# Kernel tuning notes

Measured on AMD Instinct MI355X. Metric: run time of the kernel, lower is better.

## Reference

```python
import jax, jax.numpy as jnp
import numpy as np

N = 50000
E = 800000
NFEAT, NHID, NCLASS = 128, 128, 40


def setup_inputs() -> dict:
    key = jax.random.key(0)
    ks = jax.random.split(key, 8)
    x = jax.random.normal(ks[0], (N, NFEAT), dtype=jnp.float32)
    edge_index = jax.random.randint(ks[1], (2, E), 0, N, dtype=jnp.int64)
    def glorot(k, fan_in, fan_out):
        s = jnp.sqrt(6.0 / (fan_in + fan_out)).astype(jnp.float32)
        return jax.random.uniform(k, (fan_in, fan_out), jnp.float32, -s, s)
    W1 = glorot(ks[2], NFEAT, NHID); b1 = jnp.zeros((NHID,), jnp.float32)
    W2 = glorot(ks[3], NHID, NHID);  b2 = jnp.zeros((NHID,), jnp.float32)
    W3 = glorot(ks[4], NHID, NCLASS); b3 = jnp.zeros((NCLASS,), jnp.float32)
    return {"x": x, "edge_index": edge_index,
            "W1": W1, "b1": b1, "W2": W2, "b2": b2, "W3": W3, "b3": b3}


def _gcn_norm(edge_index, num_nodes, dtype):
    # Add self-loops, then symmetric normalization D^-1/2 (A+I) D^-1/2 (PyG gcn_norm).
    loop = jnp.arange(num_nodes, dtype=edge_index.dtype)
    src = jnp.concatenate([edge_index[0], loop])
    dst = jnp.concatenate([edge_index[1], loop])
    deg = jax.ops.segment_sum(jnp.ones_like(src, dtype=dtype), dst, num_segments=num_nodes)
    dinv = jnp.where(deg > 0, deg ** -0.5, 0.0).astype(dtype)
    norm = dinv[src] * dinv[dst]  # [E+N]
    return src, dst, norm


def _gcn_conv(h, src, dst, norm, W, b, num_nodes):
    h = h @ W                              # dense transform first (out_dim small)
    msg = h[src] * norm[:, None]           # gather + per-edge scale
    out = jax.ops.segment_sum(msg, dst, num_segments=num_nodes)  # scatter-add
    return out + b


def reference(x, edge_index, W1, b1, W2, b2, W3, b3):
    src, dst, norm = _gcn_norm(edge_index, N, x.dtype)
    h = jax.nn.relu(_gcn_conv(x, src, dst, norm, W1, b1, N))  # dropout: eval mode (identity)
    h = jax.nn.relu(_gcn_conv(h, src, dst, norm, W2, b2, N))
    h = _gcn_conv(h, src, dst, norm, W3, b3, N)
    return jax.nn.log_softmax(h, axis=-1)
```

## Files before the change

kernel.cpp:

```cpp
#include <hip/hip_runtime.h>
#include <stdint.h>

#define NN 50000
#define NE 800000

#define SWZ(j, k) ((j) * 128 + ((k) ^ (((j) & 7) << 2)))

__device__ inline unsigned short f2bf(float f) {
    union { float f; uint32_t u; } x; x.f = f;
    uint32_t u = x.u;
    return (unsigned short)((u + 0x7fffu + ((u >> 16) & 1u)) >> 16);
}
__device__ inline uint32_t pack2bf(float lo, float hi) {
    return (uint32_t)f2bf(lo) | ((uint32_t)f2bf(hi) << 16);
}
__device__ inline float bf2f(unsigned short h) {
    union { uint32_t u; float f; } c; c.u = ((uint32_t)h) << 16;
    return c.f;
}
__device__ inline float2 bfp2f2(uint32_t v) {
    union { uint32_t u; float f; } a, b;
    a.u = (v & 0xffffu) << 16;
    b.u = v & 0xffff0000u;
    return make_float2(a.f, b.f);
}

#define FMA4(ACC, S, B)                  \
    ACC.x = fmaf(S, B.x, ACC.x);         \
    ACC.y = fmaf(S, B.y, ACC.y);         \
    ACC.z = fmaf(S, B.z, ACC.z);         \
    ACC.w = fmaf(S, B.w, ACC.w);


__global__ void zero_i(int* p, int n) {
    int i = blockIdx.x * blockDim.x + threadIdx.x;
    if (i < n) p[i] = 0;
}

__global__ void hist_rank(const int* __restrict__ dst, int* hist, int* rank, int e) {
    int i = blockIdx.x * blockDim.x + threadIdx.x;
    if (i < e) rank[i] = atomicAdd(hist + dst[i], 1);
}

__global__ void dinv_k(const int* __restrict__ hist, float* dinv, int n) {
    int i = blockIdx.x * blockDim.x + threadIdx.x;
    if (i < n) dinv[i] = rsqrtf(1.0f + (float)hist[i]);
}

__global__ void scan1(const int* __restrict__ hist, int* row_ptr, int* bsum, int n) {
    __shared__ int s[256];
    int tid = threadIdx.x;
    int i = blockIdx.x * 256 + tid;
    int v = (i < n) ? hist[i] : 0;
    s[tid] = v;
    __syncthreads();
#pragma unroll
    for (int off = 1; off < 256; off <<= 1) {
        int y = (tid >= off) ? s[tid - off] : 0;
        __syncthreads();
        s[tid] += y;
        __syncthreads();
    }
    if (i < n) row_ptr[i] = s[tid] - v;
    if (tid == 255) bsum[blockIdx.x] = s[255];
}

__global__ void scan2(const int* __restrict__ bsum, int* boff, int nb) {
    __shared__ int s[256];
    int tid = threadIdx.x;
    int v = (tid < nb) ? bsum[tid] : 0;
    s[tid] = v;
    __syncthreads();
#pragma unroll
    for (int off = 1; off < 256; off <<= 1) {
        int y = (tid >= off) ? s[tid - off] : 0;
        __syncthreads();
        s[tid] += y;
        __syncthreads();
    }
    if (tid < nb) boff[tid] = s[tid] - v;
}

__global__ void scan3(int* row_ptr, const int* __restrict__ boff, int n) {
    int i = blockIdx.x * blockDim.x + threadIdx.x;
    if (i < n) row_ptr[i] += boff[i >> 8];
}

__global__ void bucket(const int* __restrict__ src, const int* __restrict__ dst,
                       const int* __restrict__ row_ptr, const int* __restrict__ rank,
                       int* __restrict__ csr_src, int e) {
    int i = blockIdx.x * blockDim.x + threadIdx.x;
    if (i < e) csr_src[row_ptr[dst[i]] + rank[i]] = src[i];
}


__global__ __launch_bounds__(256) void gemm128(const float* __restrict__ X,
                                               const float* __restrict__ W,
                                               const float* __restrict__ dinv,
                                               unsigned short* __restrict__ G, int n) {
    __shared__ float Ws[128 * 128];
    int t = threadIdx.x;
    int row0 = blockIdx.x * 128;

    const float4* Wv = (const float4*)W;
    float4* Wsv = (float4*)Ws;
#pragma unroll
    for (int i = 0; i < 16; i++) Wsv[t + i * 256] = Wv[t + i * 256];
    __syncthreads();

    int tx = t & 15;
    int ty = t >> 4;

    const float* xp[8];
#pragma unroll
    for (int ri = 0; ri < 8; ri++) {
        int row = row0 + ty + 16 * ri;
        int rowc = row < n ? row : n - 1;
        xp[ri] = X + (size_t)rowc * 128;
    }

    float4 acc0[8], acc1[8];
#pragma unroll
    for (int ri = 0; ri < 8; ri++) {
        acc0[ri] = make_float4(0.f, 0.f, 0.f, 0.f);
        acc1[ri] = make_float4(0.f, 0.f, 0.f, 0.f);
    }

#pragma unroll 2
    for (int k = 0; k < 128; k += 4) {
        float4 a[8];
#pragma unroll
        for (int ri = 0; ri < 8; ri++) a[ri] = *(const float4*)(xp[ri] + k);
        float4 b0[4], b1[4];
#pragma unroll
        for (int c = 0; c < 4; c++) {
            b0[c] = *(const float4*)(&Ws[(k + c) * 128 + 4 * tx]);
            b1[c] = *(const float4*)(&Ws[(k + c) * 128 + 64 + 4 * tx]);
        }
#pragma unroll
        for (int ri = 0; ri < 8; ri++) {
            FMA4(acc0[ri], a[ri].x, b0[0]);
            FMA4(acc0[ri], a[ri].y, b0[1]);
            FMA4(acc0[ri], a[ri].z, b0[2]);
            FMA4(acc0[ri], a[ri].w, b0[3]);
            FMA4(acc1[ri], a[ri].x, b1[0]);
            FMA4(acc1[ri], a[ri].y, b1[1]);
            FMA4(acc1[ri], a[ri].z, b1[2]);
            FMA4(acc1[ri], a[ri].w, b1[3]);
        }
    }

#pragma unroll
    for (int ri = 0; ri < 8; ri++) {
        int row = row0 + ty + 16 * ri;
        if (row >= n) continue;
        float di = dinv[row];
        uint2 o0, o1;
        o0.x = pack2bf(di * acc0[ri].x, di * acc0[ri].y);
        o0.y = pack2bf(di * acc0[ri].z, di * acc0[ri].w);
        o1.x = pack2bf(di * acc1[ri].x, di * acc1[ri].y);
        o1.y = pack2bf(di * acc1[ri].z, di * acc1[ri].w);
        *(uint2*)(&G[(size_t)row * 128 + 4 * tx]) = o0;
        *(uint2*)(&G[(size_t)row * 128 + 64 + 4 * tx]) = o1;
    }
}

__global__ __launch_bounds__(256) void gemm40(const float* __restrict__ X,
                                              const float* __restrict__ W,
                                              const float* __restrict__ dinv,
                                              unsigned short* __restrict__ G, int n) {
    __shared__ float WsT[40 * 128];
    int t = threadIdx.x;
    int row0 = blockIdx.x * 128;

    const float4* Wv = (const float4*)W;
#pragma unroll
    for (int i = 0; i < 5; i++) {
        int idx = t + i * 256;
        int k = idx / 10;
        int j4 = (idx - k * 10) * 4;
        float4 v = Wv[idx];
        WsT[(j4 + 0) * 128 + (k ^ (((j4 + 0) & 7) << 2))] = v.x;
        WsT[(j4 + 1) * 128 + (k ^ (((j4 + 1) & 7) << 2))] = v.y;
        WsT[(j4 + 2) * 128 + (k ^ (((j4 + 2) & 7) << 2))] = v.z;
        WsT[(j4 + 3) * 128 + (k ^ (((j4 + 3) & 7) << 2))] = v.w;
    }
    __syncthreads();

    int tx = t & 7;
    int ty = t >> 3;

    const float* xp[4];
#pragma unroll
    for (int ri = 0; ri < 4; ri++) {
        int row = row0 + ty + 32 * ri;
        int rowc = row < n ? row : n - 1;
        xp[ri] = X + (size_t)rowc * 128;
    }

    float acc[4][5];
#pragma unroll
    for (int ri = 0; ri < 4; ri++)
#pragma unroll
        for (int ci = 0; ci < 5; ci++) acc[ri][ci] = 0.f;

#pragma unroll 2
    for (int k = 0; k < 128; k += 4) {
        float4 a[4], b[5];
#pragma unroll
        for (int ri = 0; ri < 4; ri++) a[ri] = *(const float4*)(xp[ri] + k);
#pragma unroll
        for (int ci = 0; ci < 5; ci++) b[ci] = *(const float4*)(&WsT[SWZ(tx * 5 + ci, k)]);
#pragma unroll
        for (int ri = 0; ri < 4; ri++)
#pragma unroll
            for (int ci = 0; ci < 5; ci++) {
                acc[ri][ci] = fmaf(a[ri].x, b[ci].x, acc[ri][ci]);
                acc[ri][ci] = fmaf(a[ri].y, b[ci].y, acc[ri][ci]);
                acc[ri][ci] = fmaf(a[ri].z, b[ci].z, acc[ri][ci]);
                acc[ri][ci] = fmaf(a[ri].w, b[ci].w, acc[ri][ci]);
            }
    }

#pragma unroll
    for (int ri = 0; ri < 4; ri++) {
        int row = row0 + ty + 32 * ri;
        if (row >= n) continue;
        float di = dinv[row];
#pragma unroll
        for (int ci = 0; ci < 5; ci++)
            G[(size_t)row * 40 + tx * 5 + ci] = f2bf(di * acc[ri][ci]);
    }
}


__global__ __launch_bounds__(256) void aggregate128(const unsigned short* __restrict__ G,
                                                    const int* __restrict__ row_ptr,
                                                    const int* __restrict__ hist,
                                                    const int* __restrict__ csr_src,
                                                    const float* __restrict__ dinv,
                                                    const float* __restrict__ b,
                                                    float* __restrict__ Y, int n) {
    int node = blockIdx.x * 4 + (threadIdx.x >> 6);
    if (node >= n) return;
    int l = threadIdx.x & 63;
    const uint32_t* Gr = (const uint32_t*)G;

    float2 acc = bfp2f2(Gr[(size_t)node * 64 + l]);
    int p = row_ptr[node], p1 = p + hist[node];
    for (; p + 7 < p1; p += 8) {
        int s0 = csr_src[p],     s1 = csr_src[p + 1], s2 = csr_src[p + 2], s3 = csr_src[p + 3];
        int s4 = csr_src[p + 4], s5 = csr_src[p + 5], s6 = csr_src[p + 6], s7 = csr_src[p + 7];
        uint32_t v0 = Gr[(size_t)s0 * 64 + l], v1 = Gr[(size_t)s1 * 64 + l];
        uint32_t v2 = Gr[(size_t)s2 * 64 + l], v3 = Gr[(size_t)s3 * 64 + l];
        uint32_t v4 = Gr[(size_t)s4 * 64 + l], v5 = Gr[(size_t)s5 * 64 + l];
        uint32_t v6 = Gr[(size_t)s6 * 64 + l], v7 = Gr[(size_t)s7 * 64 + l];
        float2 f0 = bfp2f2(v0), f1 = bfp2f2(v1), f2 = bfp2f2(v2), f3 = bfp2f2(v3);
        float2 f4 = bfp2f2(v4), f5 = bfp2f2(v5), f6 = bfp2f2(v6), f7 = bfp2f2(v7);
        acc.x += ((f0.x + f1.x) + (f2.x + f3.x)) + ((f4.x + f5.x) + (f6.x + f7.x));
        acc.y += ((f0.y + f1.y) + (f2.y + f3.y)) + ((f4.y + f5.y) + (f6.y + f7.y));
    }
    for (; p + 3 < p1; p += 4) {
        int s0 = csr_src[p], s1 = csr_src[p + 1], s2 = csr_src[p + 2], s3 = csr_src[p + 3];
        float2 f0 = bfp2f2(Gr[(size_t)s0 * 64 + l]), f1 = bfp2f2(Gr[(size_t)s1 * 64 + l]);
        float2 f2 = bfp2f2(Gr[(size_t)s2 * 64 + l]), f3 = bfp2f2(Gr[(size_t)s3 * 64 + l]);
        acc.x += (f0.x + f1.x) + (f2.x + f3.x);
        acc.y += (f0.y + f1.y) + (f2.y + f3.y);
    }
    for (; p < p1; ++p) {
        float2 f = bfp2f2(Gr[(size_t)csr_src[p] * 64 + l]);
        acc.x += f.x; acc.y += f.y;
    }
    float di = dinv[node];
    float vx = fmaf(di, acc.x, b[2 * l]);
    float vy = fmaf(di, acc.y, b[2 * l + 1]);
    float2 o = make_float2(vx > 0.f ? vx : 0.f, vy > 0.f ? vy : 0.f);
    *(float2*)(Y + (size_t)node * 128 + 2 * l) = o;
}

__global__ __launch_bounds__(256) void aggregate40_lsm(const unsigned short* __restrict__ G,
                                                       const int* __restrict__ row_ptr,
                                                       const int* __restrict__ hist,
                                                       const int* __restrict__ csr_src,
                                                       const float* __restrict__ dinv,
                                                       const float* __restrict__ b,
                                                       float* __restrict__ Y, int n) {
    int node = blockIdx.x * 4 + (threadIdx.x >> 6);
    if (node >= n) return;
    int lane = threadIdx.x & 63;
    bool act = lane < 40;
    int lc = act ? lane : 0;
    float acc = act ? bf2f(G[(size_t)node * 40 + lane]) : 0.f;
    int p = row_ptr[node], p1 = p + hist[node];
    for (; p + 3 < p1; p += 4) {
        int s0 = csr_src[p], s1 = csr_src[p + 1], s2 = csr_src[p + 2], s3 = csr_src[p + 3];
        float f0 = bf2f(G[(size_t)s0 * 40 + lc]);
        float f1 = bf2f(G[(size_t)s1 * 40 + lc]);
        float f2 = bf2f(G[(size_t)s2 * 40 + lc]);
        float f3 = bf2f(G[(size_t)s3 * 40 + lc]);
        acc += (f0 + f1) + (f2 + f3);
    }
    for (; p < p1; ++p) acc += bf2f(G[(size_t)csr_src[p] * 40 + lc]);

    float v = act ? fmaf(dinv[node], acc, b[lane]) : -1e30f;
    float m = v;
#pragma unroll
    for (int off = 32; off > 0; off >>= 1) m = fmaxf(m, __shfl_xor(m, off, 64));
    float ex = act ? expf(v - m) : 0.f;
    float s_ = ex;
#pragma unroll
    for (int off = 32; off > 0; off >>= 1) s_ += __shfl_xor(s_, off, 64);
    float ls = logf(s_);
    if (act) Y[(size_t)node * 40 + lane] = v - m - ls;
}


extern "C" void kernel_launch(void* const* d_in, const int* in_sizes, int n_in,
                              void* d_out, int out_size, void* d_ws, size_t ws_size,
                              hipStream_t stream) {
    const float* x  = (const float*)d_in[0];
    const int*   ei = (const int*)d_in[1];
    const float* W1 = (const float*)d_in[2];
    const float* b1 = (const float*)d_in[3];
    const float* W2 = (const float*)d_in[4];
    const float* b2 = (const float*)d_in[5];
    const float* W3 = (const float*)d_in[6];
    const float* b3 = (const float*)d_in[7];
    float* out = (float*)d_out;

    const int n = NN, e = NE;
    const int* srcI = ei;
    const int* dstI = ei + e;

    char* ws = (char*)d_ws;
    int*   hist    = (int*)ws;
    float* dinv    = (float*)(ws + 200704);
    int*   row_ptr = (int*)(ws + 401408);
    int*   bsum    = (int*)(ws + 602112);
    int*   boff    = (int*)(ws + 603136);
    int*   rank    = (int*)(ws + 604160);
    int*   csr_src = (int*)(ws + 3804160);
    unsigned short* bufG = (unsigned short*)(ws + 7004160);
    float* bufA    = (float*)(ws + 7004160 + 12800000);

    int nb = (n + 255) / 256;

    zero_i<<<nb, 256, 0, stream>>>(hist, n);
    hist_rank<<<(e + 255) / 256, 256, 0, stream>>>(dstI, hist, rank, e);
    dinv_k<<<nb, 256, 0, stream>>>(hist, dinv, n);
    scan1<<<nb, 256, 0, stream>>>(hist, row_ptr, bsum, n);
    scan2<<<1, 256, 0, stream>>>(bsum, boff, nb);
    scan3<<<nb, 256, 0, stream>>>(row_ptr, boff, n);
    bucket<<<(e + 255) / 256, 256, 0, stream>>>(srcI, dstI, row_ptr, rank, csr_src, e);

    unsigned gg = (unsigned)((n + 127) / 128);
    unsigned ga = (unsigned)((n + 3) / 4);

    gemm128<<<gg, 256, 0, stream>>>(x, W1, dinv, bufG, n);
    aggregate128<<<ga, 256, 0, stream>>>(bufG, row_ptr, hist, csr_src, dinv, b1, bufA, n);
    gemm128<<<gg, 256, 0, stream>>>(bufA, W2, dinv, bufG, n);
    aggregate128<<<ga, 256, 0, stream>>>(bufG, row_ptr, hist, csr_src, dinv, b2, bufA, n);
    gemm40<<<gg, 256, 0, stream>>>(bufA, W3, dinv, bufG, n);
    aggregate40_lsm<<<ga, 256, 0, stream>>>(bufG, row_ptr, hist, csr_src, dinv, b3, out, n);
}
```

Baseline: 322.7 us.

## Gather neighbor rows with 16-byte loads across lane groups and fuse prep kernels

Aggregation for the 128-wide layers now splits each wave into four 16-lane groups. Each group gathers a different edge's full bf16 row with 16-byte vector loads, and the partial sums are reduced across groups with shuffles. The self-loop is folded in as edge zero. The dinv computation is merged into the first scan kernel, and the block-offset add of the third scan is folded into its consumers, removing two launches. This aims for wider memory transactions and more edges in flight, at the cost of extra shuffle reductions and more predicated work on low-degree nodes.

```diff
diff --git a/kernel.cpp b/kernel.cpp
--- a/kernel.cpp
+++ b/kernel.cpp
@@ -42,12 +42,8 @@
     if (i < e) rank[i] = atomicAdd(hist + dst[i], 1);
 }
 
-__global__ void dinv_k(const int* __restrict__ hist, float* dinv, int n) {
-    int i = blockIdx.x * blockDim.x + threadIdx.x;
-    if (i < n) dinv[i] = rsqrtf(1.0f + (float)hist[i]);
-}
-
-__global__ void scan1(const int* __restrict__ hist, int* row_ptr, int* bsum, int n) {
+__global__ void scan1(const int* __restrict__ hist, int* row_ptr, int* bsum,
+                      float* dinv, int n) {
     __shared__ int s[256];
     int tid = threadIdx.x;
     int i = blockIdx.x * 256 + tid;
@@ -61,7 +57,10 @@
         s[tid] += y;
         __syncthreads();
     }
-    if (i < n) row_ptr[i] = s[tid] - v;
+    if (i < n) {
+        row_ptr[i] = s[tid] - v;
+        dinv[i] = rsqrtf(1.0f + (float)v);
+    }
     if (tid == 255) bsum[blockIdx.x] = s[255];
 }
 
@@ -81,16 +80,14 @@
     if (tid < nb) boff[tid] = s[tid] - v;
 }
 
-__global__ void scan3(int* row_ptr, const int* __restrict__ boff, int n) {
+__global__ void bucket(const int* __restrict__ src, const int* __restrict__ dst,
+                       const int* __restrict__ row_ptr, const int* __restrict__ boff,
+                       const int* __restrict__ rank, int* __restrict__ csr_src, int e) {
     int i = blockIdx.x * blockDim.x + threadIdx.x;
-    if (i < n) row_ptr[i] += boff[i >> 8];
-}
-
-__global__ void bucket(const int* __restrict__ src, const int* __restrict__ dst,
-                       const int* __restrict__ row_ptr, const int* __restrict__ rank,
-                       int* __restrict__ csr_src, int e) {
-    int i = blockIdx.x * blockDim.x + threadIdx.x;
-    if (i < e) csr_src[row_ptr[dst[i]] + rank[i]] = src[i];
+    if (i < e) {
+        int d = dst[i];
+        csr_src[row_ptr[d] + boff[d >> 8] + rank[i]] = src[i];
+    }
 }
 
 
@@ -233,9 +230,9 @@
     }
 }
 
-
 __global__ __launch_bounds__(256) void aggregate128(const unsigned short* __restrict__ G,
                                                     const int* __restrict__ row_ptr,
+                                                    const int* __restrict__ boff,
                                                     const int* __restrict__ hist,
                                                     const int* __restrict__ csr_src,
                                                     const float* __restrict__ dinv,
@@ -243,43 +240,61 @@
                                                     float* __restrict__ Y, int n) {
     int node = blockIdx.x * 4 + (threadIdx.x >> 6);
     if (node >= n) return;
-    int l = threadIdx.x & 63;
-    const uint32_t* Gr = (const uint32_t*)G;
-
-    float2 acc = bfp2f2(Gr[(size_t)node * 64 + l]);
-    int p = row_ptr[node], p1 = p + hist[node];
-    for (; p + 7 < p1; p += 8) {
-        int s0 = csr_src[p],     s1 = csr_src[p + 1], s2 = csr_src[p + 2], s3 = csr_src[p + 3];
-        int s4 = csr_src[p + 4], s5 = csr_src[p + 5], s6 = csr_src[p + 6], s7 = csr_src[p + 7];
-        uint32_t v0 = Gr[(size_t)s0 * 64 + l], v1 = Gr[(size_t)s1 * 64 + l];
-        uint32_t v2 = Gr[(size_t)s2 * 64 + l], v3 = Gr[(size_t)s3 * 64 + l];
-        uint32_t v4 = Gr[(size_t)s4 * 64 + l], v5 = Gr[(size_t)s5 * 64 + l];
-        uint32_t v6 = Gr[(size_t)s6 * 64 + l], v7 = Gr[(size_t)s7 * 64 + l];
-        float2 f0 = bfp2f2(v0), f1 = bfp2f2(v1), f2 = bfp2f2(v2), f3 = bfp2f2(v3);
-        float2 f4 = bfp2f2(v4), f5 = bfp2f2(v5), f6 = bfp2f2(v6), f7 = bfp2f2(v7);
-        acc.x += ((f0.x + f1.x) + (f2.x + f3.x)) + ((f4.x + f5.x) + (f6.x + f7.x));
-        acc.y += ((f0.y + f1.y) + (f2.y + f3.y)) + ((f4.y + f5.y) + (f6.y + f7.y));
-    }
-    for (; p + 3 < p1; p += 4) {
-        int s0 = csr_src[p], s1 = csr_src[p + 1], s2 = csr_src[p + 2], s3 = csr_src[p + 3];
-        float2 f0 = bfp2f2(Gr[(size_t)s0 * 64 + l]), f1 = bfp2f2(Gr[(size_t)s1 * 64 + l]);
-        float2 f2 = bfp2f2(Gr[(size_t)s2 * 64 + l]), f3 = bfp2f2(Gr[(size_t)s3 * 64 + l]);
-        acc.x += (f0.x + f1.x) + (f2.x + f3.x);
-        acc.y += (f0.y + f1.y) + (f2.y + f3.y);
-    }
-    for (; p < p1; ++p) {
-        float2 f = bfp2f2(Gr[(size_t)csr_src[p] * 64 + l]);
-        acc.x += f.x; acc.y += f.y;
-    }
+    int lane = threadIdx.x & 63;
+    int grp = lane >> 4;
+    int fl = lane & 15;
+    const uint4* Gq = (const uint4*)G;
+
+    float2 a0 = make_float2(0.f, 0.f), a1 = a0, a2 = a0, a3 = a0;
+    int p = row_ptr[node] + boff[node >> 8];
+    int cnt = hist[node] + 1;
+
+    for (int j = 0; j < cnt; j += 8) {
+        int e0 = j + grp, e1 = e0 + 4;
+        bool v0 = e0 < cnt, v1 = e1 < cnt;
+        int i0 = 0, i1 = 0;
+        if (v0) i0 = (e0 == 0) ? node : csr_src[p + e0 - 1];
+        if (v1) i1 = csr_src[p + e1 - 1];
+        uint4 u0, u1;
+        if (v0) u0 = Gq[(size_t)i0 * 16 + fl];
+        if (v1) u1 = Gq[(size_t)i1 * 16 + fl];
+        if (v0) {
+            float2 f;
+            f = bfp2f2(u0.x); a0.x += f.x; a0.y += f.y;
+            f = bfp2f2(u0.y); a1.x += f.x; a1.y += f.y;
+            f = bfp2f2(u0.z); a2.x += f.x; a2.y += f.y;
+            f = bfp2f2(u0.w); a3.x += f.x; a3.y += f.y;
+        }
+        if (v1) {
+            float2 f;
+            f = bfp2f2(u1.x); a0.x += f.x; a0.y += f.y;
+            f = bfp2f2(u1.y); a1.x += f.x; a1.y += f.y;
+            f = bfp2f2(u1.z); a2.x += f.x; a2.y += f.y;
+            f = bfp2f2(u1.w); a3.x += f.x; a3.y += f.y;
+        }
+    }
+
+#pragma unroll
+    for (int m = 16; m <= 32; m <<= 1) {
+        a0.x += __shfl_xor(a0.x, m, 64); a0.y += __shfl_xor(a0.y, m, 64);
+        a1.x += __shfl_xor(a1.x, m, 64); a1.y += __shfl_xor(a1.y, m, 64);
+        a2.x += __shfl_xor(a2.x, m, 64); a2.y += __shfl_xor(a2.y, m, 64);
+        a3.x += __shfl_xor(a3.x, m, 64); a3.y += __shfl_xor(a3.y, m, 64);
+    }
+
+    float2 w = grp < 2 ? (grp == 0 ? a0 : a1) : (grp == 2 ? a2 : a3);
+    int f0 = fl * 8 + grp * 2;
     float di = dinv[node];
-    float vx = fmaf(di, acc.x, b[2 * l]);
-    float vy = fmaf(di, acc.y, b[2 * l + 1]);
+    float2 bb = *(const float2*)(b + f0);
+    float vx = fmaf(di, w.x, bb.x);
+    float vy = fmaf(di, w.y, bb.y);
     float2 o = make_float2(vx > 0.f ? vx : 0.f, vy > 0.f ? vy : 0.f);
-    *(float2*)(Y + (size_t)node * 128 + 2 * l) = o;
+    *(float2*)(Y + (size_t)node * 128 + f0) = o;
 }
 
 __global__ __launch_bounds__(256) void aggregate40_lsm(const unsigned short* __restrict__ G,
                                                        const int* __restrict__ row_ptr,
+                                                       const int* __restrict__ boff,
                                                        const int* __restrict__ hist,
                                                        const int* __restrict__ csr_src,
                                                        const float* __restrict__ dinv,
@@ -291,7 +306,8 @@
     bool act = lane < 40;
     int lc = act ? lane : 0;
     float acc = act ? bf2f(G[(size_t)node * 40 + lane]) : 0.f;
-    int p = row_ptr[node], p1 = p + hist[node];
+    int p = row_ptr[node] + boff[node >> 8];
+    int p1 = p + hist[node];
     for (; p + 3 < p1; p += 4) {
         int s0 = csr_src[p], s1 = csr_src[p + 1], s2 = csr_src[p + 2], s3 = csr_src[p + 3];
         float f0 = bf2f(G[(size_t)s0 * 40 + lc]);
@@ -347,19 +363,17 @@
 
     zero_i<<<nb, 256, 0, stream>>>(hist, n);
     hist_rank<<<(e + 255) / 256, 256, 0, stream>>>(dstI, hist, rank, e);
-    dinv_k<<<nb, 256, 0, stream>>>(hist, dinv, n);
-    scan1<<<nb, 256, 0, stream>>>(hist, row_ptr, bsum, n);
+    scan1<<<nb, 256, 0, stream>>>(hist, row_ptr, bsum, dinv, n);
     scan2<<<1, 256, 0, stream>>>(bsum, boff, nb);
-    scan3<<<nb, 256, 0, stream>>>(row_ptr, boff, n);
-    bucket<<<(e + 255) / 256, 256, 0, stream>>>(srcI, dstI, row_ptr, rank, csr_src, e);
+    bucket<<<(e + 255) / 256, 256, 0, stream>>>(srcI, dstI, row_ptr, boff, rank, csr_src, e);
 
     unsigned gg = (unsigned)((n + 127) / 128);
     unsigned ga = (unsigned)((n + 3) / 4);
 
     gemm128<<<gg, 256, 0, stream>>>(x, W1, dinv, bufG, n);
-    aggregate128<<<ga, 256, 0, stream>>>(bufG, row_ptr, hist, csr_src, dinv, b1, bufA, n);
+    aggregate128<<<ga, 256, 0, stream>>>(bufG, row_ptr, boff, hist, csr_src, dinv, b1, bufA, n);
     gemm128<<<gg, 256, 0, stream>>>(bufA, W2, dinv, bufG, n);
-    aggregate128<<<ga, 256, 0, stream>>>(bufG, row_ptr, hist, csr_src, dinv, b2, bufA, n);
+    aggregate128<<<ga, 256, 0, stream>>>(bufG, row_ptr, boff, hist, csr_src, dinv, b2, bufA, n);
     gemm40<<<gg, 256, 0, stream>>>(bufA, W3, dinv, bufG, n);
-    aggregate40_lsm<<<ga, 256, 0, stream>>>(bufG, row_ptr, hist, csr_src, dinv, b3, out, n);
-}
+    aggregate40_lsm<<<ga, 256, 0, stream>>>(bufG, row_ptr, boff, hist, csr_src, dinv, b3, out, n);
+}
```

After: 328.8 us. About the same (+1.9%).
